# Kernel tuning notes

Hardware: AMD Instinct MI355X
Metric: run time of the kernel (lower is better)

## Reference

```python
import jax, jax.numpy as jnp
import numpy as np
from jax import lax

B, S, E, H = 8, 1024, 1024, 16
HEAD_DIM = E // H
THRESHOLD = 0.5
NEG_FILL = -1e9


def setup_inputs() -> dict:
    key = jax.random.key(0)
    k0, k1, k2 = jax.random.split(key, 3)
    x = jax.random.normal(k0, (B, S, E), jnp.float32)
    in_proj_w = jax.random.normal(k1, (3 * E, E), jnp.float32) * 0.02
    in_proj_b = jnp.zeros((3 * E,), jnp.float32)
    out_proj_w = jax.random.normal(k2, (E, E), jnp.float32) * 0.02
    out_proj_b = jnp.zeros((E,), jnp.float32)
    return {"x": x, "in_proj_w": in_proj_w, "in_proj_b": in_proj_b,
            "out_proj_w": out_proj_w, "out_proj_b": out_proj_b}


def _mha(x, in_proj_w, in_proj_b, out_proj_w, out_proj_b):
    # PyTorch nn.MultiheadAttention with q=k=v=x, batch_first=True
    qkv = x @ in_proj_w.T + in_proj_b                     # [B,S,3E]
    q, k, v = jnp.split(qkv, 3, axis=-1)                  # each [B,S,E]
    def split_heads(t):
        return t.reshape(B, S, H, HEAD_DIM).transpose(0, 2, 1, 3)  # [B,H,S,d]
    q, k, v = split_heads(q), split_heads(k), split_heads(v)
    scale = 1.0 / np.sqrt(HEAD_DIM).astype(np.float32)
    scores = jnp.einsum('bhqd,bhkd->bhqk', q, k) * scale  # [B,H,S,S]
    w = jax.nn.softmax(scores, axis=-1)
    o = jnp.einsum('bhqk,bhkd->bhqd', w, v)               # [B,H,S,d]
    o = o.transpose(0, 2, 1, 3).reshape(B, S, E)
    attn_output = o @ out_proj_w.T + out_proj_b           # [B,S,E]
    attn_weights = w.mean(axis=1)                         # head-averaged [B,S,S]
    return attn_output, attn_weights


def _cluster(attn_weights):
    # Sequential greedy clustering: scan rows i in order; if row i is not yet
    # visited, its high-attention columns (> THRESHOLD) form cluster i and are
    # marked visited. cluster_id[b, j] = row index of the first cluster that
    # claimed token j, or -1 if never claimed.
    visited0 = jnp.zeros((B, S), dtype=bool)
    cid0 = jnp.full((B, S), -1, dtype=jnp.int32)

    def step(carry, i):
        visited, cid = carry
        process = ~jnp.take(visited, i, axis=1)           # [B] row i unvisited?
        high = jnp.take(attn_weights, i, axis=1) > THRESHOLD  # [B,S]
        claimed = process[:, None] & high                 # [B,S]
        newly = claimed & (~visited)
        cid = jnp.where(newly, jnp.int32(i), cid)
        visited = visited | claimed
        return (visited, cid), None

    (visited, cid), _ = lax.scan(step, (visited0, cid0), jnp.arange(S))
    return cid, visited


def reference(x, in_proj_w, in_proj_b, out_proj_w, out_proj_b):
    attn_output, attn_weights = _mha(x, in_proj_w, in_proj_b, out_proj_w, out_proj_b)
    cluster_ids, covered = _cluster(attn_weights)
    # _generate_image_features: x where token belongs to some cluster, -1e9 else
    clustered_outputs = jnp.where(covered[..., None], x, jnp.float32(NEG_FILL))
    return attn_output, attn_weights, clustered_outputs, cluster_ids
```

## Files before the change

kernel.cpp:

```cpp
#include <hip/hip_runtime.h>
#include <hip/hip_bf16.h>

#define B 8
#define S 1024
#define E 1024
#define H 16

typedef unsigned short u16;
typedef unsigned char u8;
typedef unsigned int u32;
typedef unsigned long long u64;

typedef __attribute__((ext_vector_type(8))) short s16x8;
typedef __attribute__((ext_vector_type(4))) float f32x4;
typedef __attribute__((ext_vector_type(16))) float f32x16;

__device__ __forceinline__ float bf2f(u16 u) {
    union { u32 i; float f; } x; x.i = ((u32)u) << 16; return x.f;
}
__device__ __forceinline__ u16 f2bf(float f) {
    union { float f; u32 i; } x; x.f = f;
    u32 r = x.i + 0x7FFFu + ((x.i >> 16) & 1u);
    return (u16)(r >> 16);
}
__device__ __forceinline__ f32x16 zero16() {
    f32x16 z;
#pragma unroll
    for (int i = 0; i < 16; ++i) z[i] = 0.f;
    return z;
}
__device__ __forceinline__ void gload16(const u16* g, u16* l) {
    __builtin_amdgcn_global_load_lds(
        (const __attribute__((address_space(1))) u32*)g,
        (__attribute__((address_space(3))) u32*)l, 16, 0, 0);
}

__global__ __launch_bounds__(256) void cvt_all(
    const float* __restrict__ x, const float* __restrict__ w0,
    const float* __restrict__ w1, u16* __restrict__ xb,
    u16* __restrict__ wb0, u16* __restrict__ wb1) {
    int i = blockIdx.x * 256 + threadIdx.x;
    const float* src;
    u16* dst;
    int off;
    if (i < 2097152) { src = x; dst = xb; off = i; }
    else if (i < 2883584) { src = w0; dst = wb0; off = i - 2097152; }
    else { src = w1; dst = wb1; off = i - 2883584; }
    float4 v = ((const float4*)src)[off];
    union { u16 u[4]; ushort4 s; } p;
    p.u[0] = f2bf(v.x); p.u[1] = f2bf(v.y);
    p.u[2] = f2bf(v.z); p.u[3] = f2bf(v.w);
    ((ushort4*)dst)[off] = p.s;
}

template <int MODE>
__global__ __launch_bounds__(256) void mfma_gemm(
    const u16* __restrict__ A, const u16* __restrict__ W,
    const float* __restrict__ bias, u16* __restrict__ qb, u16* __restrict__ kb,
    u16* __restrict__ vt, float* __restrict__ outf) {
    __shared__ __align__(16) u16 smem[16384];
    u16* As = smem;
    u16* Bs = smem + 8192;
    const int t = threadIdx.x;
    const int lane = t & 63;
    const int w = t >> 6;
    const int tot = (int)(gridDim.x * gridDim.y);
    const int lin = (int)(blockIdx.y * gridDim.x + blockIdx.x);
    const int cpx = tot >> 3;
    const int sw = (lin & 7) * cpx + (lin >> 3);
    const int m0 = (sw & 63) * 128;
    const int n0 = (sw >> 6) * 128;
    const int wm = w >> 1, wn = w & 1;
    const int l15 = lane & 15, l4 = lane >> 4;
    const int lr = lane >> 3;
    const int lc = ((lane & 7) ^ lr) * 8;

    f32x4 acc[4][4];
#pragma unroll
    for (int i = 0; i < 4; ++i)
#pragma unroll
        for (int j = 0; j < 4; ++j) acc[i][j] = {0.f, 0.f, 0.f, 0.f};

    for (int k0 = 0; k0 < 1024; k0 += 64) {
        __syncthreads();
#pragma unroll
        for (int jj = 0; jj < 4; ++jj) {
            int j = w * 4 + jj;
            gload16(A + (size_t)(m0 + j * 8 + lr) * 1024 + k0 + lc, As + j * 512);
            gload16(W + (size_t)(n0 + j * 8 + lr) * 1024 + k0 + lc, Bs + j * 512);
        }
        __syncthreads();
#pragma unroll
        for (int ks = 0; ks < 2; ++ks) {
            s16x8 af[4], bf[4];
#pragma unroll
            for (int i = 0; i < 4; ++i) {
                int row = wm * 64 + i * 16 + l15;
                af[i] = *(const s16x8*)((const u8*)As +
                        (((row << 7) + (ks << 6) + (l4 << 4)) ^ ((row & 7) << 4)));
            }
#pragma unroll
            for (int j = 0; j < 4; ++j) {
                int row = wn * 64 + j * 16 + l15;
                bf[j] = *(const s16x8*)((const u8*)Bs +
                        (((row << 7) + (ks << 6) + (l4 << 4)) ^ ((row & 7) << 4)));
            }
#pragma unroll
            for (int i = 0; i < 4; ++i)
#pragma unroll
                for (int j = 0; j < 4; ++j)
                    acc[i][j] = __builtin_amdgcn_mfma_f32_16x16x32_bf16(
                        af[i], bf[j], acc[i][j], 0, 0, 0);
        }
    }

    if (MODE == 0) {
        __syncthreads();
        u16* Cs = smem;
        const int seg = n0 >> 10;
        const int bb = m0 >> 10;
        const int ms = m0 & 1023;
        if (seg < 2) {
            const float sc = (seg == 0) ? 0.18033688011f : 1.0f;
#pragma unroll
            for (int j = 0; j < 4; ++j) {
                int nl = wn * 64 + j * 16 + l15;
                float bn = bias[n0 + nl];
#pragma unroll
                for (int i = 0; i < 4; ++i) {
                    int ml = wm * 64 + i * 16 + l4 * 4;
#pragma unroll
                    for (int rr = 0; rr < 4; ++rr)
                        Cs[(ml + rr) * 128 + nl] = f2bf((acc[i][j][rr] + bn) * sc);
                }
            }
            __syncthreads();
            u16* dst0 = (seg == 0) ? qb : kb;
#pragma unroll
            for (int it = 0; it < 8; ++it) {
                int flat = it * 256 + t;
                int ml = flat >> 4;
                int g = (flat >> 3) & 1;
                int c8 = flat & 7;
                int hh = ((n0 + g * 64) & 1023) >> 6;
                u16* dst = dst0 + (((size_t)(bb * 16 + hh) * 1024 + ms + ml) << 6) + c8 * 8;
                *(uint4*)dst = *(const uint4*)(Cs + ml * 128 + g * 64 + c8 * 8);
            }
        } else {
#pragma unroll
            for (int j = 0; j < 4; ++j) {
                int nl = wn * 64 + j * 16 + l15;
                float bn = bias[n0 + nl];
                int sz = (nl & 7) << 4;
#pragma unroll
                for (int i = 0; i < 4; ++i) {
                    int ml = wm * 64 + i * 16 + l4 * 4;
#pragma unroll
                    for (int rr = 0; rr < 4; ++rr) {
                        int bl = (ml + rr) << 1;
                        *(u16*)((u8*)Cs + (nl << 8) + (bl ^ sz)) =
                            f2bf(acc[i][j][rr] + bn);
                    }
                }
            }
            __syncthreads();
#pragma unroll
            for (int it = 0; it < 8; ++it) {
                int flat = it * 256 + t;
                int nl = flat >> 4;
                int c = flat & 15;
                int n = n0 + nl;
                int hh = (n & 1023) >> 6;
                int d = n & 63;
                u16* dst = vt + ((size_t)(bb * 16 + hh) * 64 + d) * 1024 + ms + c * 8;
                *(uint4*)dst = *(const uint4*)((u8*)Cs + (nl << 8) +
                                               ((c << 4) ^ ((nl & 7) << 4)));
            }
        }
    } else {
#pragma unroll
        for (int j = 0; j < 4; ++j) {
            int n = n0 + wn * 64 + j * 16 + l15;
            float bn = bias[n];
#pragma unroll
            for (int i = 0; i < 4; ++i) {
                int mbase = m0 + wm * 64 + i * 16 + l4 * 4;
#pragma unroll
                for (int rr = 0; rr < 4; ++rr)
                    outf[(size_t)(mbase + rr) * 1024 + n] = acc[i][j][rr] + bn;
            }
        }
    }
}

template <int BASE>
__device__ __forceinline__ s16x8 build_pa(f32x16 e) {
    u32 a, bv, c, d;
    asm("v_cvt_pk_bf16_f32 %0, %1, %2" : "=v"(a) : "v"(e[BASE + 0]), "v"(e[BASE + 1]));
    asm("v_cvt_pk_bf16_f32 %0, %1, %2" : "=v"(bv) : "v"(e[BASE + 2]), "v"(e[BASE + 3]));
    asm("v_cvt_pk_bf16_f32 %0, %1, %2" : "=v"(c) : "v"(e[BASE + 4]), "v"(e[BASE + 5]));
    asm("v_cvt_pk_bf16_f32 %0, %1, %2" : "=v"(d) : "v"(e[BASE + 6]), "v"(e[BASE + 7]));
    asm("v_permlane32_swap_b32 %0, %1" : "+v"(a), "+v"(c));
    asm("v_permlane32_swap_b32 %0, %1" : "+v"(bv), "+v"(d));
    union { u32 w[4]; s16x8 v; } u;
    u.w[0] = a; u.w[1] = bv; u.w[2] = c; u.w[3] = d;
    return u.v;
}
__device__ __forceinline__ float pair_max(float v) {
    float a_ = v, b_ = v;
    asm("v_permlane32_swap_b32 %0, %1" : "+v"(a_), "+v"(b_));
    return fmaxf(a_, b_);
}
__device__ __forceinline__ float pair_sum(float v) {
    float a_ = v, b_ = v;
    asm("v_permlane32_swap_b32 %0, %1" : "+v"(a_), "+v"(b_));
    return a_ + b_;
}
__device__ __forceinline__ u32 pair_or(u32 v) {
    u32 a_ = v, b_ = v;
    asm("v_permlane32_swap_b32 %0, %1" : "+v"(a_), "+v"(b_));
    return a_ | b_;
}

__global__ __launch_bounds__(256, 4) void attn_flash(
    const u16* __restrict__ qg, const u16* __restrict__ kg,
    const u16* __restrict__ vtg, u16* __restrict__ og,
    float* __restrict__ stats) {
    __shared__ __align__(16) u16 bufK[2][64 * 64];
    __shared__ __align__(16) u16 bufV[2][64 * 64];
    const int t = threadIdx.x;
    const int lane = t & 63;
    const int w = t >> 6;
    const int task = ((blockIdx.x & 7) << 7) | (blockIdx.x >> 3);
    const int b = task >> 7;
    const int h = (task >> 3) & 15;
    const int qg_ = task & 7;
    const int q = lane & 31;
    const int hi = lane >> 5;
    const int q0 = qg_ * 128 + w * 32;
    const size_t hb = (size_t)(b * 16 + h) << 16;

    const int lr = lane >> 3;
    const int lc = ((lane & 7) ^ lr) * 8;
    const int swz = (q & 7) << 4;

#define STAGE(tt, bb)                                                          \
    do {                                                                       \
        _Pragma("unroll") for (int jj = 0; jj < 2; ++jj) {                     \
            int j = w * 2 + jj;                                                \
            gload16(kg + hb + (size_t)((tt) * 64 + j * 8 + lr) * 64 + lc,      \
                    bufK[bb] + j * 512);                                       \
            gload16(vtg + hb + (size_t)(j * 8 + lr) * 1024 + (tt) * 64 + lc,   \
                    bufV[bb] + j * 512);                                       \
        }                                                                      \
    } while (0)

    s16x8 qf[4];
#pragma unroll
    for (int s = 0; s < 4; ++s)
        qf[s] = *(const s16x8*)(qg + hb + (size_t)(q0 + q) * 64 + s * 16 + hi * 8);

    f32x16 oLo = zero16(), oHi = zero16();
    float m = -1e30f, l = 0.f;

    STAGE(0, 0);
    __syncthreads();
    int cur = 0;

    for (int tile = 0; tile < 16; ++tile) {
        if (tile < 15) STAGE(tile + 1, cur ^ 1);
        const u16* bK = bufK[cur];
        const u16* bV = bufV[cur];
#pragma unroll
        for (int kk = 0; kk < 64; kk += 32) {
            s16x8 ka[4];
#pragma unroll
            for (int s = 0; s < 4; ++s)
                ka[s] = *(const s16x8*)((const u8*)bK +
                        ((((kk + q) << 7) + (s << 5) + (hi << 4)) ^ swz));
            f32x16 s_ = zero16();
#pragma unroll
            for (int s = 0; s < 4; ++s)
                s_ = __builtin_amdgcn_mfma_f32_32x32x16_bf16(ka[s], qf[s], s_, 0, 0, 0);
            float m0 = fmaxf(fmaxf(s_[0], s_[4]), fmaxf(s_[8], s_[12]));
            float m1 = fmaxf(fmaxf(s_[1], s_[5]), fmaxf(s_[9], s_[13]));
            float m2 = fmaxf(fmaxf(s_[2], s_[6]), fmaxf(s_[10], s_[14]));
            float m3 = fmaxf(fmaxf(s_[3], s_[7]), fmaxf(s_[11], s_[15]));
            float pmax = pair_max(fmaxf(fmaxf(m0, m1), fmaxf(m2, m3)));
            if (__any(pmax > m + 11.5f)) {
                float mn = fmaxf(m, pmax);
                float r = exp2f(m - mn);
                m = mn;
                l *= r;
                oLo = oLo * r;
                oHi = oHi * r;
            }
            float s0 = 0.f, s1 = 0.f, s2 = 0.f, s3 = 0.f;
#pragma unroll
            for (int i = 0; i < 16; i += 4) {
                s_[i + 0] = exp2f(s_[i + 0] - m);
                s_[i + 1] = exp2f(s_[i + 1] - m);
                s_[i + 2] = exp2f(s_[i + 2] - m);
                s_[i + 3] = exp2f(s_[i + 3] - m);
                s0 += s_[i + 0]; s1 += s_[i + 1]; s2 += s_[i + 2]; s3 += s_[i + 3];
            }
            l += pair_sum((s0 + s1) + (s2 + s3));
            s16x8 p0 = build_pa<0>(s_), p1 = build_pa<8>(s_);
            s16x8 vLo0 = *(const s16x8*)((const u8*)bV +
                         (((q << 7) + (kk << 1) + (hi << 4)) ^ swz));
            s16x8 vLo1 = *(const s16x8*)((const u8*)bV +
                         (((q << 7) + (kk << 1) + 32 + (hi << 4)) ^ swz));
            s16x8 vHi0 = *(const s16x8*)((const u8*)bV +
                         ((((q + 32) << 7) + (kk << 1) + (hi << 4)) ^ swz));
            s16x8 vHi1 = *(const s16x8*)((const u8*)bV +
                         ((((q + 32) << 7) + (kk << 1) + 32 + (hi << 4)) ^ swz));
            oLo = __builtin_amdgcn_mfma_f32_32x32x16_bf16(vLo0, p0, oLo, 0, 0, 0);
            oLo = __builtin_amdgcn_mfma_f32_32x32x16_bf16(vLo1, p1, oLo, 0, 0, 0);
            oHi = __builtin_amdgcn_mfma_f32_32x32x16_bf16(vHi0, p0, oHi, 0, 0, 0);
            oHi = __builtin_amdgcn_mfma_f32_32x32x16_bf16(vHi1, p1, oHi, 0, 0, 0);
        }
        __syncthreads();
        cur ^= 1;
    }
#undef STAGE
    float inv = 1.0f / l;
    oLo = oLo * inv;
    oHi = oHi * inv;
    u16* orow = og + (size_t)(b * 1024 + q0 + q) * 1024 + h * 64;
#pragma unroll
    for (int rg = 0; rg < 4; ++rg) {
        union { u16 u[4]; u64 v; } pk;
#pragma unroll
        for (int j = 0; j < 4; ++j) pk.u[j] = f2bf(oLo[4 * rg + j]);
        *(u64*)(orow + 8 * rg + 4 * hi) = pk.v;
#pragma unroll
        for (int j = 0; j < 4; ++j) pk.u[j] = f2bf(oHi[4 * rg + j]);
        *(u64*)(orow + 32 + 4 * hi + 8 * rg) = pk.v;
    }
    if (hi == 0)
        stats[(size_t)(b * 16 + h) * 1024 + q0 + q] = m + 4.0f + log2f(l);
}

__global__ __launch_bounds__(256, 3) void attn_aw(
    const u16* __restrict__ qg, const u16* __restrict__ kg,
    const float* __restrict__ stats, float* __restrict__ aw,
    u64* __restrict__ maskg) {
    __shared__ __align__(16) u16 bufK[2][64 * 64];
    __shared__ __align__(16) u16 bufQ[2][128 * 64];
    const int t = threadIdx.x;
    const int lane = t & 63;
    const int w = t >> 6;
    const int sw = ((blockIdx.x & 7) << 7) | (blockIdx.x >> 3);
    const int b = sw >> 7;
    const int ks = (sw >> 3) & 15;
    const int qg_ = sw & 7;
    const int q = lane & 31;
    const int hi = lane >> 5;
    const int q0 = qg_ * 128;
    const int qr = w * 32 + q;
    const int kbase = ks * 64;

    const int lr = lane >> 3;
    const int lc = ((lane & 7) ^ lr) * 8;
    const int swz = (q & 7) << 4;

#define STAGEAW(hh, bb)                                                        \
    do {                                                                       \
        const size_t hbs = (size_t)(b * 16 + (hh)) << 16;                      \
        _Pragma("unroll") for (int jj = 0; jj < 2; ++jj) {                     \
            int j = w * 2 + jj;                                                \
            gload16(kg + hbs + (size_t)(kbase + j * 8 + lr) * 64 + lc,         \
                    bufK[bb] + j * 512);                                       \
        }                                                                      \
        _Pragma("unroll") for (int jj = 0; jj < 4; ++jj) {                     \
            int j = w * 4 + jj;                                                \
            gload16(qg + hbs + (size_t)(q0 + j * 8 + lr) * 64 + lc,            \
                    bufQ[bb] + j * 512);                                       \
        }                                                                      \
    } while (0)

    f32x16 awA = zero16(), awB = zero16();

    STAGEAW(0, 0);
    __syncthreads();
    int cur = 0;

    for (int h = 0; h < 16; ++h) {
        if (h < 15) STAGEAW(h + 1, cur ^ 1);
        const u16* bK = bufK[cur];
        const u16* bQ = bufQ[cur];
        s16x8 qf[4], kA[4], kB[4];
#pragma unroll
        for (int s = 0; s < 4; ++s) {
            qf[s] = *(const s16x8*)((const u8*)bQ +
                    (((qr << 7) + (s << 5) + (hi << 4)) ^ swz));
            kA[s] = *(const s16x8*)((const u8*)bK +
                    (((q << 7) + (s << 5) + (hi << 4)) ^ swz));
            kB[s] = *(const s16x8*)((const u8*)bK +
                    ((((q + 32) << 7) + (s << 5) + (hi << 4)) ^ swz));
        }
        float C = stats[(size_t)(b * 16 + h) * 1024 + q0 + qr];
        f32x16 sA = zero16(), sB = zero16();
#pragma unroll
        for (int s = 0; s < 4; ++s) {
            sA = __builtin_amdgcn_mfma_f32_32x32x16_bf16(kA[s], qf[s], sA, 0, 0, 0);
            sB = __builtin_amdgcn_mfma_f32_32x32x16_bf16(kB[s], qf[s], sB, 0, 0, 0);
        }
#pragma unroll
        for (int i = 0; i < 16; ++i) {
            awA[i] += exp2f(sA[i] - C);
            awB[i] += exp2f(sB[i] - C);
        }
        __syncthreads();
        cur ^= 1;
    }
#undef STAGEAW
    float* awrow = aw + (size_t)(b * 1024 + q0 + qr) * 1024 + kbase;
#pragma unroll
    for (int rg = 0; rg < 4; ++rg) {
        *(float4*)(awrow + 8 * rg + 4 * hi) =
            make_float4(awA[4 * rg + 0], awA[4 * rg + 1], awA[4 * rg + 2], awA[4 * rg + 3]);
        *(float4*)(awrow + 32 + 8 * rg + 4 * hi) =
            make_float4(awB[4 * rg + 0], awB[4 * rg + 1], awB[4 * rg + 2], awB[4 * rg + 3]);
    }
    u32 lo = 0, hi32 = 0;
#pragma unroll
    for (int r = 0; r < 16; ++r) {
        int k = (r & 3) + 8 * (r >> 2) + 4 * hi;
        lo |= (awA[r] > 0.5f) ? (1u << k) : 0u;
        hi32 |= (awB[r] > 0.5f) ? (1u << k) : 0u;
    }
    lo = pair_or(lo);
    hi32 = pair_or(hi32);
    if (hi == 0)
        maskg[(size_t)(b * 1024 + q0 + qr) * 16 + ks] = ((u64)hi32 << 32) | (u64)lo;
}

__global__ __launch_bounds__(256) void cluster_kernel(
    const u64* __restrict__ maskg, float* __restrict__ cid, u64* __restrict__ cov) {
    __shared__ u64 mask[16384];
    __shared__ u16 rows[1024];
    const int t = threadIdx.x;
    const int b = blockIdx.x;
#pragma unroll
    for (int i = 0; i < 64; ++i)
        mask[t + 256 * i] = maskg[(size_t)b * 16384 + t + 256 * i];
#pragma unroll
    for (int i = 0; i < 4; ++i) cid[b * S + t + 256 * i] = -1.0f;
    __syncthreads();
    if (t < 64) {
        int nr = 0;
        for (int it = 0; it < 16; ++it) {
            int row = it * 64 + t;
            const u64* mp = mask + row * 16;
            u64 orv = 0;
#pragma unroll
            for (int j = 0; j < 16; ++j) orv |= mp[j];
            u64 bal = __ballot(orv != 0ULL);
            int pre = __popcll(bal & ((1ULL << t) - 1ULL));
            if (orv != 0ULL) rows[nr + pre] = (u16)row;
            nr += __popcll(bal);
        }
        u64 vis = 0;
        for (int idx = 0; idx < nr; ++idx) {
            int i = rows[idx];
            u64 viw = __shfl(vis, i >> 6);
            bool proc = ((viw >> (i & 63)) & 1ULL) == 0ULL;
            u64 cl = (proc && t < 16) ? mask[i * 16 + t] : 0ULL;
            u64 newly = cl & ~vis;
            vis |= cl;
            while (newly) {
                int bit = __ffsll((long long)newly) - 1;
                cid[b * S + t * 64 + bit] = (float)i;
                newly &= newly - 1;
            }
        }
        if (t < 16) cov[b * 16 + t] = vis;
    }
}

__global__ __launch_bounds__(256) void clustered_kernel(
    const float* __restrict__ x, const u64* __restrict__ cov,
    float* __restrict__ out2) {
    const size_t n4 = (size_t)B * S * E / 4;
    size_t idx = (size_t)blockIdx.x * 256 + threadIdx.x;
    const float4 neg = make_float4(-1e9f, -1e9f, -1e9f, -1e9f);
    for (; idx < n4; idx += (size_t)gridDim.x * 256) {
        size_t tok = idx >> 8;
        int bb = (int)(tok >> 10), s = (int)(tok & 1023);
        u64 m = cov[bb * 16 + (s >> 6)];
        bool c = ((m >> (s & 63)) & 1ULL) != 0ULL;
        float4 v = ((const float4*)x)[idx];
        ((float4*)out2)[idx] = c ? v : neg;
    }
}

extern "C" void kernel_launch(void* const* d_in, const int* in_sizes, int n_in,
                              void* d_out, int out_size, void* d_ws, size_t ws_size,
                              hipStream_t stream) {
    const float* x = (const float*)d_in[0];
    const float* w_in = (const float*)d_in[1];
    const float* b_in = (const float*)d_in[2];
    const float* w_out = (const float*)d_in[3];
    const float* b_out = (const float*)d_in[4];

    float* out0 = (float*)d_out;
    float* out1 = out0 + 8388608;
    float* out2 = out1 + 8388608;
    float* out3 = out2 + 8388608;

    u16* q_bf = (u16*)out0;
    u16* vt_bf = q_bf + 8388608;
    u16* xb = (u16*)out1;
    u16* k_bf = (u16*)out2;
    u16* wb0 = k_bf + 8388608;
    u16* wb1 = wb0 + 3145728;
    float* statsF = (float*)(k_bf + 12582912);
    u16* o_bf = (u16*)d_ws;
    u64* maskg = (u64*)((char*)d_ws + (size_t)(16u << 20));
    u64* cov = (u64*)((char*)d_ws + (size_t)(17u << 20));

    cvt_all<<<12288, 256, 0, stream>>>(x, w_in, w_out, xb, wb0, wb1);

    mfma_gemm<0><<<dim3(64, 24), 256, 0, stream>>>(xb, wb0, b_in, q_bf, k_bf,
                                                   vt_bf, nullptr);
    attn_flash<<<1024, 256, 0, stream>>>(q_bf, k_bf, vt_bf, o_bf, statsF);
    attn_aw<<<1024, 256, 0, stream>>>(q_bf, k_bf, statsF, out1, maskg);
    mfma_gemm<1><<<dim3(64, 8), 256, 0, stream>>>(o_bf, wb1, b_out, nullptr,
                                                  nullptr, nullptr, out0);

    cluster_kernel<<<8, 256, 0, stream>>>(maskg, out3, cov);
    clustered_kernel<<<2048, 256, 0, stream>>>(x, cov, out2);
}
```

Measured before the change: 252.4 us.

## Enlarge attn_aw tile to 128x128 and remap GEMM tiles per XCD

Measured after the change: 258.8 us. 1.03x slower.

```diff
diff --git a/kernel.cpp b/kernel.cpp
--- a/kernel.cpp
+++ b/kernel.cpp
@@ -64,12 +64,14 @@
     const int t = threadIdx.x;
     const int lane = t & 63;
     const int w = t >> 6;
-    const int tot = (int)(gridDim.x * gridDim.y);
     const int lin = (int)(blockIdx.y * gridDim.x + blockIdx.x);
-    const int cpx = tot >> 3;
-    const int sw = (lin & 7) * cpx + (lin >> 3);
-    const int m0 = (sw & 63) * 128;
-    const int n0 = (sw >> 6) * 128;
+    const int xcd = lin & 7;
+    const int idx = lin >> 3;
+    int mt, nt;
+    if (MODE == 0) { mt = (xcd & 3) * 16 + (idx & 15); nt = (xcd >> 2) * 12 + (idx >> 4); }
+    else           { mt = xcd * 8 + (idx & 7);         nt = idx >> 3; }
+    const int m0 = mt * 128;
+    const int n0 = nt * 128;
     const int wm = w >> 1, wn = w & 1;
     const int l15 = lane & 15, l4 = lane >> 4;
     const int lr = lane >> 3;
@@ -341,24 +343,27 @@
         stats[(size_t)(b * 16 + h) * 1024 + q0 + q] = m + 4.0f + log2f(l);
 }
 
-__global__ __launch_bounds__(256, 3) void attn_aw(
+__global__ __launch_bounds__(512, 2) void attn_aw(
     const u16* __restrict__ qg, const u16* __restrict__ kg,
     const float* __restrict__ stats, float* __restrict__ aw,
     u64* __restrict__ maskg) {
-    __shared__ __align__(16) u16 bufK[2][64 * 64];
+    __shared__ __align__(16) u16 bufK[2][128 * 64];
     __shared__ __align__(16) u16 bufQ[2][128 * 64];
     const int t = threadIdx.x;
     const int lane = t & 63;
     const int w = t >> 6;
-    const int sw = ((blockIdx.x & 7) << 7) | (blockIdx.x >> 3);
-    const int b = sw >> 7;
-    const int ks = (sw >> 3) & 15;
-    const int qg_ = sw & 7;
+    const int task = ((blockIdx.x & 7) << 6) | (blockIdx.x >> 3);
+    const int b = task >> 6;
+    const int ks = (task >> 3) & 7;
+    const int qg_ = task & 7;
     const int q = lane & 31;
     const int hi = lane >> 5;
+    const int wq = w >> 1;
+    const int kh = w & 1;
     const int q0 = qg_ * 128;
-    const int qr = w * 32 + q;
-    const int kbase = ks * 64;
+    const int qr = wq * 32 + q;
+    const int krow0 = kh * 64;
+    const int kbase = ks * 128 + kh * 64;
 
     const int lr = lane >> 3;
     const int lc = ((lane & 7) ^ lr) * 8;
@@ -368,12 +373,9 @@
     do {                                                                       \
         const size_t hbs = (size_t)(b * 16 + (hh)) << 16;                      \
         _Pragma("unroll") for (int jj = 0; jj < 2; ++jj) {                     \
-            int j = w * 2 + jj;                                                \
-            gload16(kg + hbs + (size_t)(kbase + j * 8 + lr) * 64 + lc,         \
+            int j = w * 2 + jj;                        \
+            gload16(kg + hbs + (size_t)(ks * 128 + j * 8 + lr) * 64 + lc,      \
                     bufK[bb] + j * 512);                                       \
-        }                                                                      \
-        _Pragma("unroll") for (int jj = 0; jj < 4; ++jj) {                     \
-            int j = w * 4 + jj;                                                \
             gload16(qg + hbs + (size_t)(q0 + j * 8 + lr) * 64 + lc,            \
                     bufQ[bb] + j * 512);                                       \
         }                                                                      \
@@ -395,9 +397,9 @@
             qf[s] = *(const s16x8*)((const u8*)bQ +
                     (((qr << 7) + (s << 5) + (hi << 4)) ^ swz));
             kA[s] = *(const s16x8*)((const u8*)bK +
-                    (((q << 7) + (s << 5) + (hi << 4)) ^ swz));
+                    ((((krow0 + q) << 7) + (s << 5) + (hi << 4)) ^ swz));
             kB[s] = *(const s16x8*)((const u8*)bK +
-                    ((((q + 32) << 7) + (s << 5) + (hi << 4)) ^ swz));
+                    ((((krow0 + q + 32) << 7) + (s << 5) + (hi << 4)) ^ swz));
         }
         float C = stats[(size_t)(b * 16 + h) * 1024 + q0 + qr];
         f32x16 sA = zero16(), sB = zero16();
@@ -433,7 +435,8 @@
     lo = pair_or(lo);
     hi32 = pair_or(hi32);
     if (hi == 0)
-        maskg[(size_t)(b * 1024 + q0 + qr) * 16 + ks] = ((u64)hi32 << 32) | (u64)lo;
+        maskg[(size_t)(b * 1024 + q0 + qr) * 16 + ks * 2 + kh] =
+            ((u64)hi32 << 32) | (u64)lo;
 }
 
 __global__ __launch_bounds__(256) void cluster_kernel(
@@ -525,7 +528,7 @@
     mfma_gemm<0><<<dim3(64, 24), 256, 0, stream>>>(xb, wb0, b_in, q_bf, k_bf,
                                                    vt_bf, nullptr);
     attn_flash<<<1024, 256, 0, stream>>>(q_bf, k_bf, vt_bf, o_bf, statsF);
-    attn_aw<<<1024, 256, 0, stream>>>(q_bf, k_bf, statsF, out1, maskg);
+    attn_aw<<<512, 512, 0, stream>>>(q_bf, k_bf, statsF, out1, maskg);
     mfma_gemm<1><<<dim3(64, 8), 256, 0, stream>>>(o_bf, wb1, b_out, nullptr,
                                                   nullptr, nullptr, out0);
 
```
